# Performance work log

Measured on AMD Instinct MI355X. Metric: run time of the kernel, lower is better.

Reference implementation:

```python
import jax, jax.numpy as jnp
import numpy as np

EMB_DIM = 256
ATT_DIM = 256
B, S = 8, 2048


def setup_inputs() -> dict:
    key = jax.random.key(0)
    ks = jax.random.split(key, 9)
    scale = 1.0 / np.sqrt(EMB_DIM)
    inp = {
        "x": jax.random.normal(ks[0], (B, S, EMB_DIM), dtype=jnp.float32),
        "mask": jax.random.randint(ks[1], (B, S, S), 0, 2, dtype=jnp.int32),
        "Wq": jax.random.uniform(ks[2], (EMB_DIM, ATT_DIM), jnp.float32, -scale, scale),
        "bq": jax.random.uniform(ks[3], (ATT_DIM,), jnp.float32, -scale, scale),
        "Wk": jax.random.uniform(ks[4], (EMB_DIM, ATT_DIM), jnp.float32, -scale, scale),
        "bk": jax.random.uniform(ks[5], (ATT_DIM,), jnp.float32, -scale, scale),
        "Wv": jax.random.uniform(ks[6], (EMB_DIM, ATT_DIM), jnp.float32, -scale, scale),
        "bv": jax.random.uniform(ks[7], (ATT_DIM,), jnp.float32, -scale, scale),
    }
    return inp


def reference(x, mask, Wq, bq, Wk, bk, Wv, bv):
    # Linear projections: (B,S,E) @ (E,A) + (A,)
    q = jnp.einsum("bse,ea->bsa", x, Wq) + bq
    k = jnp.einsum("bse,ea->bsa", x, Wk) + bk
    v = jnp.einsum("bse,ea->bsa", x, Wv) + bv
    # scores: (B,S,S)
    scores = jnp.einsum("bqa,bka->bqk", q, k) / jnp.sqrt(jnp.float32(ATT_DIM))
    scores = jnp.where(mask == 0, jnp.float32(-1e9), scores)
    attn = jax.nn.softmax(scores, axis=-1)
    return jnp.einsum("bqk,bka->bqa", attn, v)
```

## Files before the change

### kernel.cpp

```cpp
#include <hip/hip_runtime.h>
#include <hip/hip_bf16.h>
#include <stdint.h>

#define BATCH 8
#define SEQ   2048
#define EMB   256
#define ADIM  256

typedef __bf16 bf16_t;
typedef __attribute__((ext_vector_type(8))) __bf16 bf16x8;
typedef __attribute__((ext_vector_type(4))) float  f32x4;
typedef uint32_t u32;
typedef unsigned long long u64;

static __device__ __forceinline__ f32x4 mfma16(bf16x8 a, bf16x8 b, f32x4 c) {
    return __builtin_amdgcn_mfma_f32_16x16x32_bf16(a, b, c, 0, 0, 0);
}

static __device__ __forceinline__ void gld16(const void* g, void* l) {
    __builtin_amdgcn_global_load_lds((const __attribute__((address_space(1))) u32*)g,
                                     (__attribute__((address_space(3))) u32*)l, 16, 0, 0);
}
static __device__ __forceinline__ void gld4(const void* g, void* l) {
    __builtin_amdgcn_global_load_lds((const __attribute__((address_space(1))) u32*)g,
                                     (__attribute__((address_space(3))) u32*)l, 4, 0, 0);
}

__global__ __launch_bounds__(256) void pack_linear(const int* msk, u32* tmp,
                                                   long el0, long nchunk, long stride) {
    long gw = (long)blockIdx.x * 4 + (threadIdx.x >> 6);
    int lane = threadIdx.x & 63;
    for (long c = gw; c < nchunk; c += stride) {
        long el = el0 + c * 64;
        int v = msk[el + lane];
        u64 b = __ballot(v != 0);
        if (lane == 0)  tmp[2 * c]     = (u32)b;
        if (lane == 32) tmp[2 * c + 1] = (u32)(b >> 32);
    }
}

__global__ __launch_bounds__(256) void pack_direct(const int* msk, u32* pm,
                                                   long el0, long nchunk, long stride) {
    long gw = (long)blockIdx.x * 4 + (threadIdx.x >> 6);
    int lane = threadIdx.x & 63;
    for (long c = gw; c < nchunk; c += stride) {
        long el = el0 + c * 64;
        int v = msk[el + lane];
        u64 b = __ballot(v != 0);
        long bb  = el >> 22;
        long rem = el & 4194303L;
        long s   = rem >> 11;
        long w0  = (rem & 2047) >> 5;
        long d0  = (bb * 64 + w0) * 2048 + s;
        if (lane == 0)  pm[d0]        = (u32)b;
        if (lane == 32) pm[d0 + 2048] = (u32)(b >> 32);
    }
}

__global__ __launch_bounds__(256) void pack_fix(const u32* tmp_tail, const u32* tmp_a, u32* pm) {
    int t = blockIdx.x * 256 + threadIdx.x;
    if (t < 32768) {
        long c = t >> 1; int half = t & 1;
        long w = (c & 31) * 2 + half;
        long s = c >> 5;
        pm[w * 2048 + s] = tmp_tail[t];
    } else if (t < 33792) {
        int t2 = t - 32768;
        long c2 = t2 >> 1; int half = t2 & 1;
        long w = (c2 & 31) * 2 + half;
        long s = 2032 + (c2 >> 5);
        pm[(7 * 64 + w) * 2048 + s] = tmp_a[t2];
    }
}

__global__ __launch_bounds__(256, 2) void proj_kv(const float* __restrict__ x,
                                                  const float* __restrict__ Wk,
                                                  const float* __restrict__ Wv,
                                                  const float* __restrict__ bk,
                                                  const float* __restrict__ bv,
                                                  char* __restrict__ Ksw,
                                                  char* __restrict__ Vsw) {
    __shared__ __align__(16) char Ws[32768];
    const int tid  = threadIdx.x;
    const int wid  = tid >> 6;
    const int lane = tid & 63;
    const int lq   = lane >> 4;
    const int ln   = lane & 15;
    const int wp   = blockIdx.x & 1;
    const int mbase = (blockIdx.x >> 1) * 64 + wid * 16;
    const float* W    = wp ? Wv : Wk;
    const float* bias = wp ? bv : bk;

    bf16x8 xf[8];
    const float* xp = x + (size_t)(mbase + ln) * EMB;
    #pragma unroll
    for (int c = 0; c < 8; ++c) {
        f32x4 a = *(const f32x4*)(xp + c * 32 + lq * 8);
        f32x4 b = *(const f32x4*)(xp + c * 32 + lq * 8 + 4);
        bf16x8 v;
        v[0] = (bf16_t)a[0]; v[1] = (bf16_t)a[1]; v[2] = (bf16_t)a[2]; v[3] = (bf16_t)a[3];
        v[4] = (bf16_t)b[0]; v[5] = (bf16_t)b[1]; v[6] = (bf16_t)b[2]; v[7] = (bf16_t)b[3];
        xf[c] = v;
    }

    f32x4 acc[16];
    #pragma unroll
    for (int t = 0; t < 16; ++t) acc[t] = (f32x4){0.f, 0.f, 0.f, 0.f};

    const int e = ln & 7;
    #pragma unroll 1
    for (int cp = 0; cp < 8; ++cp) {
        __syncthreads();
        {
            const float* wpp = W + (size_t)(cp * 32) * 256 + tid;
            #pragma unroll
            for (int i = 0; i < 4; ++i) {
                bf16x8 pk;
                #pragma unroll
                for (int j = 0; j < 8; ++j)
                    pk[j] = (bf16_t)wpp[(size_t)(i * 8 + j) * 256];
                *(bf16x8*)(Ws + tid * 128 + ((i ^ (tid & 7)) * 16)) = pk;
            }
        }
        __syncthreads();
        #pragma unroll
        for (int t = 0; t < 16; ++t) {
            bf16x8 wf = *(const bf16x8*)(Ws + (t * 16 + ln) * 128 + ((lq ^ e) * 16));
            acc[t] = mfma16(xf[cp], wf, acc[t]);
        }
    }

    if (wp == 0) {
        #pragma unroll
        for (int t = 0; t < 16; ++t) {
            float bb = bias[t * 16 + ln];
            int cb = t * 2 + (ln >> 3);
            int j  = ln & 7;
            #pragma unroll
            for (int r = 0; r < 4; ++r) {
                int s = mbase + lq * 4 + r;
                int b = s >> 11, sb = s & 2047;
                int tile = sb >> 5, n = sb & 31;
                *(bf16_t*)(Ksw + (size_t)b * 1048576 + tile * 16384 + n * 512 +
                           (((cb ^ (n & 7))) * 16) + j * 2) = (bf16_t)(acc[t][r] + bb);
            }
        }
    } else {
        const int vswz_l = (ln & 3) ^ ((ln >> 2) & 3);
        #pragma unroll
        for (int t = 0; t < 16; ++t) {
            float bb = bias[t * 16 + ln];
            int a = t * 16 + ln;
            #pragma unroll
            for (int r = 0; r < 4; ++r) {
                int s = mbase + lq * 4 + r;
                int b = s >> 11, sb = s & 2047;
                int tile = sb >> 5, k = sb & 31;
                int lqv = k >> 3, j = k & 7;
                *(bf16_t*)(Vsw + (size_t)b * 1048576 + tile * 16384 + a * 64 +
                           ((lqv ^ vswz_l) * 16) + j * 2) = (bf16_t)(acc[t][r] + bb);
            }
        }
    }
}

__global__ __launch_bounds__(256, 1) void flash_kernel(const float* __restrict__ x,
                                                       const float* __restrict__ WqM,
                                                       const float* __restrict__ bq,
                                                       const char* __restrict__ Ksw,
                                                       const char* __restrict__ Vsw,
                                                       const u32* __restrict__ pm,
                                                       float* __restrict__ out) {
    __shared__ __align__(16) char smem[71680];
    const int tid  = threadIdx.x;
    const int wid  = tid >> 6;
    const int lane = tid & 63;
    const int lq   = lane >> 4;
    const int ln   = lane & 15;
    const int qw   = wid >> 1;
    const int kw   = wid & 1;
    const int batch = blockIdx.x & 7;
    const int qbase = (blockIdx.x >> 3) * 64;

    const char* Kb = Ksw + (size_t)batch * 1048576;
    const char* Vb = Vsw + (size_t)batch * 1048576;
    char* Pq_ = smem + 65536 + qw * 2560;
    char* Pt  = smem + 65536 + wid * 1280;
    char* pmS = smem + 70656;
    float* Ls = (float*)(smem + 71168);

    {
        const char* kg = Kb + wid * 4096 + lane * 16;
        const char* vg = Vb + wid * 4096 + lane * 16;
        char* kl = smem + wid * 4096;
        char* vl = smem + 16384 + wid * 4096;
        #pragma unroll
        for (int i = 0; i < 4; ++i) gld16(kg + i * 1024, kl + i * 1024);
        #pragma unroll
        for (int i = 0; i < 4; ++i) gld16(vg + i * 1024, vl + i * 1024);
        if (wid == 0) gld4(pm + (size_t)(batch * 64 + 0) * 2048 + qbase + lane, pmS);
    }

    bf16x8 qf[2][8];
    {
        bf16x8 xf[2][8];
        #pragma unroll
        for (int h = 0; h < 2; ++h) {
            const float* xp = x + (size_t)(batch * SEQ + qbase + qw * 32 + h * 16 + ln) * EMB;
            #pragma unroll
            for (int c = 0; c < 8; ++c) {
                f32x4 a = *(const f32x4*)(xp + c * 32 + lq * 8);
                f32x4 b = *(const f32x4*)(xp + c * 32 + lq * 8 + 4);
                bf16x8 v;
                v[0] = (bf16_t)a[0]; v[1] = (bf16_t)a[1]; v[2] = (bf16_t)a[2]; v[3] = (bf16_t)a[3];
                v[4] = (bf16_t)b[0]; v[5] = (bf16_t)b[1]; v[6] = (bf16_t)b[2]; v[7] = (bf16_t)b[3];
                xf[h][c] = v;
            }
        }
        f32x4 qacc[2][16];
        #pragma unroll
        for (int h = 0; h < 2; ++h)
            #pragma unroll
            for (int t = 0; t < 16; ++t) qacc[h][t] = (f32x4){0.f, 0.f, 0.f, 0.f};

        char* Wsp = smem + 32768;
        const int e = ln & 7;
        #pragma unroll 1
        for (int cp = 0; cp < 8; ++cp) {
            __syncthreads();
            const float* wqp = WqM + (size_t)(cp * 32) * 256 + tid;
            #pragma unroll
            for (int i = 0; i < 4; ++i) {
                bf16x8 pk;
                #pragma unroll
                for (int j = 0; j < 8; ++j)
                    pk[j] = (bf16_t)wqp[(size_t)(i * 8 + j) * 256];
                *(bf16x8*)(Wsp + tid * 128 + ((i ^ (tid & 7)) * 16)) = pk;
            }
            __syncthreads();
            #pragma unroll
            for (int t = 0; t < 16; ++t) {
                bf16x8 wf = *(const bf16x8*)(Wsp + (t * 16 + ln) * 128 + ((lq ^ e) * 16));
                qacc[0][t] = mfma16(xf[0][cp], wf, qacc[0][t]);
                qacc[1][t] = mfma16(xf[1][cp], wf, qacc[1][t]);
            }
        }
        #pragma unroll
        for (int h = 0; h < 2; ++h) {
            #pragma unroll
            for (int c = 0; c < 8; ++c) {
                #pragma unroll
                for (int half = 0; half < 2; ++half) {
                    int t = 2 * c + half;
                    float bb = bq[t * 16 + ln];
                    #pragma unroll
                    for (int r = 0; r < 4; ++r) {
                        float v = (qacc[h][t][r] + bb) * 0.0625f;
                        ((bf16_t*)(Pt + (lq * 4 + r) * 80))[half * 16 + ln] = (bf16_t)v;
                    }
                }
                qf[h][c] = *(const bf16x8*)(Pt + ln * 80 + lq * 16);
            }
        }
    }

    f32x4 o[2][8];
    #pragma unroll
    for (int h = 0; h < 2; ++h)
        #pragma unroll
        for (int t = 0; t < 8; ++t) o[h][t] = (f32x4){0.f, 0.f, 0.f, 0.f};
    float lsum[2][4] = {{0.f,0.f,0.f,0.f},{0.f,0.f,0.f,0.f}};

    const int bitpos = kw * 16 + ln;
    const int kswz   = ln & 7;
    const int vswz   = (lq ^ (ln & 3) ^ ((ln >> 2) & 3)) * 16;
    const int n0     = kw * 16 + ln;

    for (int kt = 0; kt < 64; ++kt) {
        __syncthreads();
        if (kt + 1 < 64) {
            int nb = (kt + 1) & 1;
            const char* kg = Kb + (size_t)(kt + 1) * 16384 + wid * 4096 + lane * 16;
            const char* vg = Vb + (size_t)(kt + 1) * 16384 + wid * 4096 + lane * 16;
            char* kl = smem + nb * 32768 + wid * 4096;
            char* vl = smem + nb * 32768 + 16384 + wid * 4096;
            #pragma unroll
            for (int i = 0; i < 4; ++i) gld16(kg + i * 1024, kl + i * 1024);
            #pragma unroll
            for (int i = 0; i < 4; ++i) gld16(vg + i * 1024, vl + i * 1024);
            if (wid == 0)
                gld4(pm + (size_t)(batch * 64 + kt + 1) * 2048 + qbase + lane, pmS + nb * 256);
        }
        const int buf = kt & 1;
        const char* Ksb = smem + buf * 32768;
        const char* Vsb = smem + buf * 32768 + 16384;

        f32x4 s0 = (f32x4){0.f,0.f,0.f,0.f};
        f32x4 s1 = (f32x4){0.f,0.f,0.f,0.f};
        const char* krow = Ksb + n0 * 512;
        #pragma unroll
        for (int c = 0; c < 8; ++c) {
            bf16x8 kf = *(const bf16x8*)(krow + (((c * 4 + lq) ^ kswz) * 16));
            s0 = mfma16(qf[0][c], kf, s0);
            s1 = mfma16(qf[1][c], kf, s1);
        }

        u32 pw0[4], pw1[4];
        *(uint4*)pw0 = *(const uint4*)(pmS + buf * 256 + (qw * 32 + lq * 4) * 4);
        *(uint4*)pw1 = *(const uint4*)(pmS + buf * 256 + (qw * 32 + 16 + lq * 4) * 4);

        #pragma unroll
        for (int r = 0; r < 4; ++r) {
            float p0 = ((pw0[r] >> bitpos) & 1u) ? __expf(s0[r]) : 0.f;
            float p1 = ((pw1[r] >> bitpos) & 1u) ? __expf(s1[r]) : 0.f;
            lsum[0][r] += p0;
            lsum[1][r] += p1;
            ((bf16_t*)(Pq_ + (lq * 4 + r) * 80))[kw * 16 + ln]        = (bf16_t)p0;
            ((bf16_t*)(Pq_ + (16 + lq * 4 + r) * 80))[kw * 16 + ln]   = (bf16_t)p1;
        }

        asm volatile("s_waitcnt lgkmcnt(0)\n\ts_barrier" ::: "memory");

        bf16x8 pa0 = *(const bf16x8*)(Pq_ + ln * 80 + lq * 16);
        bf16x8 pa1 = *(const bf16x8*)(Pq_ + (16 + ln) * 80 + lq * 16);

        const char* vbase = Vsb + (kw * 128 + ln) * 64 + vswz;
        #pragma unroll
        for (int t = 0; t < 8; ++t) {
            bf16x8 vf = *(const bf16x8*)(vbase + t * 1024);
            o[0][t] = mfma16(pa0, vf, o[0][t]);
            o[1][t] = mfma16(pa1, vf, o[1][t]);
        }
    }

    __syncthreads();
    #pragma unroll
    for (int h = 0; h < 2; ++h) {
        #pragma unroll
        for (int r = 0; r < 4; ++r) {
            float v = lsum[h][r];
            v += __shfl_xor(v, 1);
            v += __shfl_xor(v, 2);
            v += __shfl_xor(v, 4);
            v += __shfl_xor(v, 8);
            if (ln == 0) Ls[(qw * 2 + kw) * 32 + h * 16 + lq * 4 + r] = v;
            lsum[h][r] = v;
        }
    }
    __syncthreads();
    #pragma unroll
    for (int h = 0; h < 2; ++h) {
        #pragma unroll
        for (int r = 0; r < 4; ++r) {
            int row = h * 16 + lq * 4 + r;
            float other = Ls[(qw * 2 + (1 - kw)) * 32 + row];
            float inv = 1.0f / (lsum[h][r] + other);
            float* orow = out + (size_t)(batch * SEQ + qbase + qw * 32 + row) * ADIM + kw * 128 + ln;
            #pragma unroll
            for (int t = 0; t < 8; ++t)
                orow[t * 16] = o[h][t][r] * inv;
        }
    }
}

extern "C" void kernel_launch(void* const* d_in, const int* in_sizes, int n_in,
                              void* d_out, int out_size, void* d_ws, size_t ws_size,
                              hipStream_t stream) {
    const float* x    = (const float*)d_in[0];
    int*         mask = (int*)d_in[1];
    const float* Wq   = (const float*)d_in[2];
    const float* bq   = (const float*)d_in[3];
    const float* Wk   = (const float*)d_in[4];
    const float* bk   = (const float*)d_in[5];
    const float* Wv   = (const float*)d_in[6];
    const float* bv   = (const float*)d_in[7];
    float* out = (float*)d_out;

    char* Ksw = (char*)d_ws;
    char* Vsw = Ksw + (size_t)8 * 1024 * 1024;

    u32* pm       = (u32*)mask;
    u32* tmp_tail = (u32*)mask + 33521664;
    u32* tmp_a    = (u32*)((char*)d_out + 4 * 1024 * 1024);

    pack_linear<<<128, 256, 0, stream>>>(mask, tmp_a, 33521664L, 512L, 512L);
    pack_linear<<<1024, 256, 0, stream>>>(mask, tmp_tail, 0L, 16384L, 4096L);
    pack_direct<<<2048, 256, 0, stream>>>(mask, pm, 1048576L, 507392L, 8192L);
    pack_fix<<<132, 256, 0, stream>>>(tmp_tail, tmp_a, pm);

    proj_kv<<<512, 256, 0, stream>>>(x, Wk, Wv, bk, bv, Ksw, Vsw);
    flash_kernel<<<256, 256, 0, stream>>>(x, Wq, bq, Ksw, Vsw, pm, out);
}
```

Before: 398.0 us.

## Halve flash query tile to double grid, and restructure mask bit-packing kernels

The flash attention kernel now processes 32 query rows per block instead of 64 and launches 512 blocks with launch bounds allowing two blocks per CU. This is meant to fill more of the GPU and improve latency hiding, at the cost of reloading K/V tiles twice as often per query. The mask packing is merged into fewer kernels that each load four 64-element chunks per wave iteration to raise memory-level parallelism. This uses a scratch buffer inside the output and drops the separate tail-fixup path.

Measured after the change: 409.2 us. 2.8% more time.

```diff
diff --git a/kernel.cpp b/kernel.cpp
--- a/kernel.cpp
+++ b/kernel.cpp
@@ -26,51 +26,54 @@
                                      (__attribute__((address_space(3))) u32*)l, 4, 0, 0);
 }
 
-__global__ __launch_bounds__(256) void pack_linear(const int* msk, u32* tmp,
-                                                   long el0, long nchunk, long stride) {
-    long gw = (long)blockIdx.x * 4 + (threadIdx.x >> 6);
-    int lane = threadIdx.x & 63;
-    for (long c = gw; c < nchunk; c += stride) {
-        long el = el0 + c * 64;
-        int v = msk[el + lane];
-        u64 b = __ballot(v != 0);
-        if (lane == 0)  tmp[2 * c]     = (u32)b;
-        if (lane == 32) tmp[2 * c + 1] = (u32)(b >> 32);
-    }
-}
-
-__global__ __launch_bounds__(256) void pack_direct(const int* msk, u32* pm,
-                                                   long el0, long nchunk, long stride) {
-    long gw = (long)blockIdx.x * 4 + (threadIdx.x >> 6);
-    int lane = threadIdx.x & 63;
-    for (long c = gw; c < nchunk; c += stride) {
-        long el = el0 + c * 64;
-        int v = msk[el + lane];
-        u64 b = __ballot(v != 0);
-        long bb  = el >> 22;
-        long rem = el & 4194303L;
-        long s   = rem >> 11;
-        long w0  = (rem & 2047) >> 5;
-        long d0  = (bb * 64 + w0) * 2048 + s;
-        if (lane == 0)  pm[d0]        = (u32)b;
-        if (lane == 32) pm[d0 + 2048] = (u32)(b >> 32);
-    }
-}
-
-__global__ __launch_bounds__(256) void pack_fix(const u32* tmp_tail, const u32* tmp_a, u32* pm) {
+
+__global__ __launch_bounds__(256) void pack_head(const int* __restrict__ msk,
+                                                 u32* __restrict__ tmp) {
+    const int gw   = blockIdx.x * 4 + (threadIdx.x >> 6);
+    const int lane = threadIdx.x & 63;
+    for (int c = gw; c < 4096; c += 1024) {
+        const int* mp = msk + c * 256 + lane;
+        int v0 = mp[0], v1 = mp[64], v2 = mp[128], v3 = mp[192];
+        u64 b0 = __ballot(v0 != 0), b1 = __ballot(v1 != 0),
+            b2 = __ballot(v2 != 0), b3 = __ballot(v3 != 0);
+        if (lane < 8) {
+            const int i = lane >> 1, h = lane & 1;
+            u64 bi = (i == 0) ? b0 : (i == 1) ? b1 : (i == 2) ? b2 : b3;
+            tmp[c * 8 + lane] = (u32)(bi >> (32 * h));
+        }
+    }
+}
+
+__global__ __launch_bounds__(256) void pack_bulk(const int* __restrict__ msk,
+                                                 u32* __restrict__ pm) {
+    const long gw   = (long)blockIdx.x * 4 + (threadIdx.x >> 6);
+    const int  lane = threadIdx.x & 63;
+    for (long c = gw; c < 126976; c += 4096) {
+        const long base = 1048576 + c * 256;
+        const int* mp = msk + base + lane;
+        int v0 = mp[0], v1 = mp[64], v2 = mp[128], v3 = mp[192];
+        u64 b0 = __ballot(v0 != 0), b1 = __ballot(v1 != 0),
+            b2 = __ballot(v2 != 0), b3 = __ballot(v3 != 0);
+        if (lane < 8) {
+            const int i = lane >> 1, h = lane & 1;
+            u64 bi = (i == 0) ? b0 : (i == 1) ? b1 : (i == 2) ? b2 : b3;
+            const long el64 = base + (long)i * 64;
+            const long b   = el64 >> 22;
+            const long rem = el64 & 4194303L;
+            const long s   = rem >> 11;
+            const long w0  = (rem & 2047) >> 5;
+            pm[(b * 64 + w0 + h) * 2048 + s] = (u32)(bi >> (32 * h));
+        }
+    }
+}
+
+__global__ __launch_bounds__(256) void pack_fix(const u32* __restrict__ tmp,
+                                                u32* __restrict__ pm) {
     int t = blockIdx.x * 256 + threadIdx.x;
-    if (t < 32768) {
-        long c = t >> 1; int half = t & 1;
-        long w = (c & 31) * 2 + half;
-        long s = c >> 5;
-        pm[w * 2048 + s] = tmp_tail[t];
-    } else if (t < 33792) {
-        int t2 = t - 32768;
-        long c2 = t2 >> 1; int half = t2 & 1;
-        long w = (c2 & 31) * 2 + half;
-        long s = 2032 + (c2 >> 5);
-        pm[(7 * 64 + w) * 2048 + s] = tmp_a[t2];
-    }
+    int c = t >> 1, half = t & 1;
+    int w = (c & 31) * 2 + half;
+    int s = c >> 5;
+    pm[w * 2048 + s] = tmp[t];
 }
 
 __global__ __launch_bounds__(256, 2) void proj_kv(const float* __restrict__ x,
@@ -141,7 +144,7 @@
                 int s = mbase + lq * 4 + r;
                 int b = s >> 11, sb = s & 2047;
                 int tile = sb >> 5, n = sb & 31;
-                *(bf16_t*)(Ksw + (size_t)b * 1048576 + tile * 16384 + n * 512 +
+                *(bf16_t*)(Ksw + (size_t)b * 1048576 + (size_t)tile * 16384 + n * 512 +
                            (((cb ^ (n & 7))) * 16) + j * 2) = (bf16_t)(acc[t][r] + bb);
             }
         }
@@ -157,21 +160,21 @@
                 int b = s >> 11, sb = s & 2047;
                 int tile = sb >> 5, k = sb & 31;
                 int lqv = k >> 3, j = k & 7;
-                *(bf16_t*)(Vsw + (size_t)b * 1048576 + tile * 16384 + a * 64 +
+                *(bf16_t*)(Vsw + (size_t)b * 1048576 + (size_t)tile * 16384 + a * 64 +
                            ((lqv ^ vswz_l) * 16) + j * 2) = (bf16_t)(acc[t][r] + bb);
             }
         }
     }
 }
 
-__global__ __launch_bounds__(256, 1) void flash_kernel(const float* __restrict__ x,
+__global__ __launch_bounds__(256, 2) void flash_kernel(const float* __restrict__ x,
                                                        const float* __restrict__ WqM,
                                                        const float* __restrict__ bq,
                                                        const char* __restrict__ Ksw,
                                                        const char* __restrict__ Vsw,
                                                        const u32* __restrict__ pm,
                                                        float* __restrict__ out) {
-    __shared__ __align__(16) char smem[71680];
+    __shared__ __align__(16) char smem[73984];
     const int tid  = threadIdx.x;
     const int wid  = tid >> 6;
     const int lane = tid & 63;
@@ -180,14 +183,14 @@
     const int qw   = wid >> 1;
     const int kw   = wid & 1;
     const int batch = blockIdx.x & 7;
-    const int qbase = (blockIdx.x >> 3) * 64;
+    const int qbase = (blockIdx.x >> 3) * 32;
 
     const char* Kb = Ksw + (size_t)batch * 1048576;
     const char* Vb = Vsw + (size_t)batch * 1048576;
-    char* Pq_ = smem + 65536 + qw * 2560;
-    char* Pt  = smem + 65536 + wid * 1280;
-    char* pmS = smem + 70656;
-    float* Ls = (float*)(smem + 71168);
+    char*  Pq_ = smem + 65536 + qw * 1280;
+    char*  pmS = smem + 68096;
+    float* Ls  = (float*)(smem + 68608);
+    char*  Pt  = smem + 68864 + wid * 1280;
 
     {
         const char* kg = Kb + wid * 4096 + lane * 16;
@@ -201,27 +204,22 @@
         if (wid == 0) gld4(pm + (size_t)(batch * 64 + 0) * 2048 + qbase + lane, pmS);
     }
 
-    bf16x8 qf[2][8];
+    bf16x8 qf[8];
     {
-        bf16x8 xf[2][8];
-        #pragma unroll
-        for (int h = 0; h < 2; ++h) {
-            const float* xp = x + (size_t)(batch * SEQ + qbase + qw * 32 + h * 16 + ln) * EMB;
-            #pragma unroll
-            for (int c = 0; c < 8; ++c) {
-                f32x4 a = *(const f32x4*)(xp + c * 32 + lq * 8);
-                f32x4 b = *(const f32x4*)(xp + c * 32 + lq * 8 + 4);
-                bf16x8 v;
-                v[0] = (bf16_t)a[0]; v[1] = (bf16_t)a[1]; v[2] = (bf16_t)a[2]; v[3] = (bf16_t)a[3];
-                v[4] = (bf16_t)b[0]; v[5] = (bf16_t)b[1]; v[6] = (bf16_t)b[2]; v[7] = (bf16_t)b[3];
-                xf[h][c] = v;
-            }
-        }
-        f32x4 qacc[2][16];
-        #pragma unroll
-        for (int h = 0; h < 2; ++h)
-            #pragma unroll
-            for (int t = 0; t < 16; ++t) qacc[h][t] = (f32x4){0.f, 0.f, 0.f, 0.f};
+        bf16x8 xf[8];
+        const float* xp = x + (size_t)(batch * SEQ + qbase + qw * 16 + ln) * EMB;
+        #pragma unroll
+        for (int c = 0; c < 8; ++c) {
+            f32x4 a = *(const f32x4*)(xp + c * 32 + lq * 8);
+            f32x4 b = *(const f32x4*)(xp + c * 32 + lq * 8 + 4);
+            bf16x8 v;
+            v[0] = (bf16_t)a[0]; v[1] = (bf16_t)a[1]; v[2] = (bf16_t)a[2]; v[3] = (bf16_t)a[3];
+            v[4] = (bf16_t)b[0]; v[5] = (bf16_t)b[1]; v[6] = (bf16_t)b[2]; v[7] = (bf16_t)b[3];
+            xf[c] = v;
+        }
+        f32x4 qacc[16];
+        #pragma unroll
+        for (int t = 0; t < 16; ++t) qacc[t] = (f32x4){0.f, 0.f, 0.f, 0.f};
 
         char* Wsp = smem + 32768;
         const int e = ln & 7;
@@ -241,35 +239,29 @@
             #pragma unroll
             for (int t = 0; t < 16; ++t) {
                 bf16x8 wf = *(const bf16x8*)(Wsp + (t * 16 + ln) * 128 + ((lq ^ e) * 16));
-                qacc[0][t] = mfma16(xf[0][cp], wf, qacc[0][t]);
-                qacc[1][t] = mfma16(xf[1][cp], wf, qacc[1][t]);
-            }
-        }
-        #pragma unroll
-        for (int h = 0; h < 2; ++h) {
-            #pragma unroll
-            for (int c = 0; c < 8; ++c) {
+                qacc[t] = mfma16(xf[cp], wf, qacc[t]);
+            }
+        }
+        #pragma unroll
+        for (int c = 0; c < 8; ++c) {
+            #pragma unroll
+            for (int half = 0; half < 2; ++half) {
+                int t = 2 * c + half;
+                float bb = bq[t * 16 + ln];
                 #pragma unroll
-                for (int half = 0; half < 2; ++half) {
-                    int t = 2 * c + half;
-                    float bb = bq[t * 16 + ln];
-                    #pragma unroll
-                    for (int r = 0; r < 4; ++r) {
-                        float v = (qacc[h][t][r] + bb) * 0.0625f;
-                        ((bf16_t*)(Pt + (lq * 4 + r) * 80))[half * 16 + ln] = (bf16_t)v;
-                    }
+                for (int r = 0; r < 4; ++r) {
+                    float v = (qacc[t][r] + bb) * 0.0625f;
+                    ((bf16_t*)(Pt + (lq * 4 + r) * 80))[half * 16 + ln] = (bf16_t)v;
                 }
-                qf[h][c] = *(const bf16x8*)(Pt + ln * 80 + lq * 16);
-            }
-        }
-    }
-
-    f32x4 o[2][8];
-    #pragma unroll
-    for (int h = 0; h < 2; ++h)
-        #pragma unroll
-        for (int t = 0; t < 8; ++t) o[h][t] = (f32x4){0.f, 0.f, 0.f, 0.f};
-    float lsum[2][4] = {{0.f,0.f,0.f,0.f},{0.f,0.f,0.f,0.f}};
+            }
+            qf[c] = *(const bf16x8*)(Pt + ln * 80 + lq * 16);
+        }
+    }
+
+    f32x4 o[8];
+    #pragma unroll
+    for (int t = 0; t < 8; ++t) o[t] = (f32x4){0.f, 0.f, 0.f, 0.f};
+    float lsum[4] = {0.f, 0.f, 0.f, 0.f};
 
     const int bitpos = kw * 16 + ln;
     const int kswz   = ln & 7;
@@ -295,71 +287,56 @@
         const char* Ksb = smem + buf * 32768;
         const char* Vsb = smem + buf * 32768 + 16384;
 
-        f32x4 s0 = (f32x4){0.f,0.f,0.f,0.f};
-        f32x4 s1 = (f32x4){0.f,0.f,0.f,0.f};
+        f32x4 s = (f32x4){0.f,0.f,0.f,0.f};
         const char* krow = Ksb + n0 * 512;
         #pragma unroll
         for (int c = 0; c < 8; ++c) {
             bf16x8 kf = *(const bf16x8*)(krow + (((c * 4 + lq) ^ kswz) * 16));
-            s0 = mfma16(qf[0][c], kf, s0);
-            s1 = mfma16(qf[1][c], kf, s1);
-        }
-
-        u32 pw0[4], pw1[4];
-        *(uint4*)pw0 = *(const uint4*)(pmS + buf * 256 + (qw * 32 + lq * 4) * 4);
-        *(uint4*)pw1 = *(const uint4*)(pmS + buf * 256 + (qw * 32 + 16 + lq * 4) * 4);
-
+            s = mfma16(qf[c], kf, s);
+        }
+
+        u32 pw[4];
+        *(uint4*)pw = *(const uint4*)(pmS + buf * 256 + (qw * 16 + lq * 4) * 4);
         #pragma unroll
         for (int r = 0; r < 4; ++r) {
-            float p0 = ((pw0[r] >> bitpos) & 1u) ? __expf(s0[r]) : 0.f;
-            float p1 = ((pw1[r] >> bitpos) & 1u) ? __expf(s1[r]) : 0.f;
-            lsum[0][r] += p0;
-            lsum[1][r] += p1;
-            ((bf16_t*)(Pq_ + (lq * 4 + r) * 80))[kw * 16 + ln]        = (bf16_t)p0;
-            ((bf16_t*)(Pq_ + (16 + lq * 4 + r) * 80))[kw * 16 + ln]   = (bf16_t)p1;
+            float p = ((pw[r] >> bitpos) & 1u) ? __expf(s[r]) : 0.f;
+            lsum[r] += p;
+            ((bf16_t*)(Pq_ + (lq * 4 + r) * 80))[kw * 16 + ln] = (bf16_t)p;
         }
 
         asm volatile("s_waitcnt lgkmcnt(0)\n\ts_barrier" ::: "memory");
 
-        bf16x8 pa0 = *(const bf16x8*)(Pq_ + ln * 80 + lq * 16);
-        bf16x8 pa1 = *(const bf16x8*)(Pq_ + (16 + ln) * 80 + lq * 16);
+        bf16x8 pa = *(const bf16x8*)(Pq_ + ln * 80 + lq * 16);
 
         const char* vbase = Vsb + (kw * 128 + ln) * 64 + vswz;
         #pragma unroll
         for (int t = 0; t < 8; ++t) {
             bf16x8 vf = *(const bf16x8*)(vbase + t * 1024);
-            o[0][t] = mfma16(pa0, vf, o[0][t]);
-            o[1][t] = mfma16(pa1, vf, o[1][t]);
+            o[t] = mfma16(pa, vf, o[t]);
         }
     }
 
     __syncthreads();
     #pragma unroll
-    for (int h = 0; h < 2; ++h) {
-        #pragma unroll
-        for (int r = 0; r < 4; ++r) {
-            float v = lsum[h][r];
-            v += __shfl_xor(v, 1);
-            v += __shfl_xor(v, 2);
-            v += __shfl_xor(v, 4);
-            v += __shfl_xor(v, 8);
-            if (ln == 0) Ls[(qw * 2 + kw) * 32 + h * 16 + lq * 4 + r] = v;
-            lsum[h][r] = v;
-        }
+    for (int r = 0; r < 4; ++r) {
+        float v = lsum[r];
+        v += __shfl_xor(v, 1);
+        v += __shfl_xor(v, 2);
+        v += __shfl_xor(v, 4);
+        v += __shfl_xor(v, 8);
+        if (ln == 0) Ls[(qw * 2 + kw) * 16 + lq * 4 + r] = v;
+        lsum[r] = v;
     }
     __syncthreads();
     #pragma unroll
-    for (int h = 0; h < 2; ++h) {
-        #pragma unroll
-        for (int r = 0; r < 4; ++r) {
-            int row = h * 16 + lq * 4 + r;
-            float other = Ls[(qw * 2 + (1 - kw)) * 32 + row];
-            float inv = 1.0f / (lsum[h][r] + other);
-            float* orow = out + (size_t)(batch * SEQ + qbase + qw * 32 + row) * ADIM + kw * 128 + ln;
-            #pragma unroll
-            for (int t = 0; t < 8; ++t)
-                orow[t * 16] = o[h][t][r] * inv;
-        }
+    for (int r = 0; r < 4; ++r) {
+        int row = lq * 4 + r;
+        float other = Ls[(qw * 2 + (1 - kw)) * 16 + row];
+        float inv = 1.0f / (lsum[r] + other);
+        float* orow = out + (size_t)(batch * SEQ + qbase + qw * 16 + row) * ADIM + kw * 128 + ln;
+        #pragma unroll
+        for (int t = 0; t < 8; ++t)
+            orow[t * 16] = o[t][r] * inv;
     }
 }
 
@@ -379,15 +356,12 @@
     char* Ksw = (char*)d_ws;
     char* Vsw = Ksw + (size_t)8 * 1024 * 1024;
 
-    u32* pm       = (u32*)mask;
-    u32* tmp_tail = (u32*)mask + 33521664;
-    u32* tmp_a    = (u32*)((char*)d_out + 4 * 1024 * 1024);
-
-    pack_linear<<<128, 256, 0, stream>>>(mask, tmp_a, 33521664L, 512L, 512L);
-    pack_linear<<<1024, 256, 0, stream>>>(mask, tmp_tail, 0L, 16384L, 4096L);
-    pack_direct<<<2048, 256, 0, stream>>>(mask, pm, 1048576L, 507392L, 8192L);
-    pack_fix<<<132, 256, 0, stream>>>(tmp_tail, tmp_a, pm);
-
+    u32* pm  = (u32*)mask;
+    u32* tmp = (u32*)((char*)d_out + 8 * 1024 * 1024);
+
+    pack_head<<<256, 256, 0, stream>>>(mask, tmp);
+    pack_bulk<<<1024, 256, 0, stream>>>(mask, pm);
+    pack_fix<<<128, 256, 0, stream>>>(tmp, pm);
     proj_kv<<<512, 256, 0, stream>>>(x, Wk, Wv, bk, bv, Ksw, Vsw);
-    flash_kernel<<<256, 256, 0, stream>>>(x, Wq, bq, Ksw, Vsw, pm, out);
-}
+    flash_kernel<<<512, 256, 0, stream>>>(x, Wq, bq, Ksw, Vsw, pm, out);
+}
```
